# Kernel optimization log

Measured on AMD Instinct MI355X. Metric: run time of the kernel, lower is better.

The kernel has to match this reference:

```python
import jax, jax.numpy as jnp
import numpy as np

B, T, C = 4, 2048, 1024
E, FF, TOPK = 8, 2048, 2


def setup_inputs() -> dict:
    key = jax.random.key(0)
    k1, k2, k3, k4 = jax.random.split(key, 4)
    s_in = 1.0 / np.sqrt(C)
    s_ff = 1.0 / np.sqrt(FF)
    return {
        "x": jax.random.normal(k1, (B, T, C), dtype=jnp.float32),
        "gate_w": jax.random.normal(k2, (E, C), dtype=jnp.float32) * s_in,
        "w1": jax.random.normal(k3, (E, FF, C), dtype=jnp.float32) * s_in,
        "w2": jax.random.normal(k4, (E, C, FF), dtype=jnp.float32) * s_ff,
    }


def reference(x, gate_w, w1, w2):
    Bq, Tq, Cq = x.shape
    x_flat = x.reshape(-1, Cq)                       # [N, C]
    N = x_flat.shape[0]
    scores = x_flat @ gate_w.T                       # [N, E]
    topk_scores, topk_idx = jax.lax.top_k(scores, TOPK)
    topk_probs = jax.nn.softmax(topk_scores, axis=-1)  # [N, K]
    # combine weights per expert: cw[n, e] = sum_k probs[n,k] * (idx[n,k]==e)
    cw = jnp.zeros((N, E), dtype=x_flat.dtype).at[
        jnp.arange(N)[:, None], topk_idx
    ].add(topk_probs)                                # [N, E]
    y = jnp.zeros_like(x_flat)
    for e in range(E):
        h = jax.nn.silu(x_flat @ w1[e].T) @ w2[e].T  # [N, C]
        y = y + cw[:, e:e + 1] * h
    return y.reshape(Bq, Tq, Cq)
```

## Files before the change

kernel.cpp:

```cpp
#include <hip/hip_runtime.h>
#include <hip/hip_bf16.h>
#include <math.h>

#define NTOK 8192
#define CDIM 1024
#define NEXP 8
#define FFD  2048
#define BM   128
#define RMAX (NTOK*2 + NEXP*BM)

typedef __attribute__((ext_vector_type(8))) short short8;
typedef __attribute__((ext_vector_type(4))) float f32x4;

__device__ __forceinline__ unsigned short f2b(float f){
    __hip_bfloat16 b = __float2bfloat16(f);
    return *reinterpret_cast<unsigned short*>(&b);
}
__device__ __forceinline__ float b2f(unsigned short u){
    __hip_bfloat16 b = *reinterpret_cast<__hip_bfloat16*>(&u);
    return __bfloat162float(b);
}

__device__ __forceinline__ void gl_lds16(const void* g, void* l){
    __builtin_amdgcn_global_load_lds(
        (const __attribute__((address_space(1))) unsigned int*)g,
        (__attribute__((address_space(3))) unsigned int*)l, 16, 0, 0);
}

__global__ void k_cvt(const float* __restrict__ src, unsigned short* __restrict__ dst, int n8){
    int i = blockIdx.x*blockDim.x + threadIdx.x;
    if(i >= n8) return;
    const float4* s = reinterpret_cast<const float4*>(src) + (size_t)i*2;
    float4 a = s[0], b = s[1];
    ushort4 o0 = { f2b(a.x), f2b(a.y), f2b(a.z), f2b(a.w) };
    ushort4 o1 = { f2b(b.x), f2b(b.y), f2b(b.z), f2b(b.w) };
    ushort4* d = reinterpret_cast<ushort4*>(dst) + (size_t)i*2;
    d[0] = o0; d[1] = o1;
}

__global__ void k_gate(const float* __restrict__ x, const float* __restrict__ gw,
                       unsigned short* __restrict__ Xb,
                       int* __restrict__ eidx, float* __restrict__ probs){
    int tok  = blockIdx.x*4 + (threadIdx.x>>6);
    int l    = threadIdx.x & 63;
    const float4* xr  = reinterpret_cast<const float4*>(x + (size_t)tok*CDIM);
    ushort4*      xbw = reinterpret_cast<ushort4*>(Xb + (size_t)tok*CDIM);
    float acc[NEXP];
    #pragma unroll
    for(int e=0;e<NEXP;e++) acc[e]=0.f;
    #pragma unroll
    for(int i=0;i<4;i++){
        float4 v = xr[l + 64*i];
        ushort4 o = { f2b(v.x), f2b(v.y), f2b(v.z), f2b(v.w) };
        xbw[l + 64*i] = o;
        #pragma unroll
        for(int e=0;e<NEXP;e++){
            float4 g = reinterpret_cast<const float4*>(gw + e*CDIM)[l + 64*i];
            acc[e] += v.x*g.x + v.y*g.y + v.z*g.z + v.w*g.w;
        }
    }
    #pragma unroll
    for(int e=0;e<NEXP;e++){
        #pragma unroll
        for(int off=32; off; off>>=1) acc[e] += __shfl_xor(acc[e], off);
    }
    if(l==0){
        int e0=0; float s0=acc[0];
        #pragma unroll
        for(int e=1;e<NEXP;e++) if(acc[e]>s0){s0=acc[e]; e0=e;}
        int e1=-1; float s1=-1e30f;
        #pragma unroll
        for(int e=0;e<NEXP;e++) if(e!=e0 && acc[e]>s1){s1=acc[e]; e1=e;}
        float p0 = 1.f/(1.f + expf(s1-s0));
        float p1 = 1.f - p0;
        eidx[2*tok]=e0;  eidx[2*tok+1]=e1;
        probs[2*tok]=p0; probs[2*tok+1]=p1;
    }
}

__global__ void k_rank(const int* __restrict__ eidx, int* __restrict__ slot,
                       int* __restrict__ aoff, int pad){
    __shared__ int run[NEXP];
    __shared__ int wavehist[16][NEXP];
    int tid  = threadIdx.x;
    int lane = tid & 63, w = tid >> 6;
    if(tid < NEXP) run[tid] = 0;
    __syncthreads();
    for(int iter=0; iter<(2*NTOK)/1024; iter++){
        int t = iter*1024 + tid;
        int e = eidx[t];
        unsigned long long mymask = 0;
        #pragma unroll
        for(int ee=0; ee<NEXP; ee++){
            unsigned long long m = __ballot(e==ee);
            if(ee==e) mymask = m;
            if(lane==0) wavehist[w][ee] = __popcll(m);
        }
        int lanerank = __popcll(mymask & ((1ULL<<lane)-1ULL));
        __syncthreads();
        if(tid < NEXP){
            int base = run[tid];
            #pragma unroll
            for(int ww=0; ww<16; ww++){
                int c = wavehist[ww][tid];
                wavehist[ww][tid] = base;
                base += c;
            }
            run[tid] = base;
        }
        __syncthreads();
        slot[t] = wavehist[w][e] + lanerank;
    }
    __syncthreads();
    if(tid==0){
        int off=0;
        for(int e=0;e<NEXP;e++){ aoff[e]=off; off += (run[e]+pad-1)&~(pad-1); }
        aoff[NEXP]=off;
    }
}

__global__ void k_build(const int* __restrict__ eidx, const int* __restrict__ slot,
                        const int* __restrict__ aoff,
                        int* __restrict__ tor, int* __restrict__ row_of){
    int t = blockIdx.x*blockDim.x + threadIdx.x;
    int e = eidx[t];
    int row = aoff[e] + slot[t];
    tor[row] = t>>1;
    row_of[t] = row;
}

template<int KDIM, bool GATHER, bool SILU>
__global__ __launch_bounds__(256, 4)
void k_gemm_fast(const unsigned short* __restrict__ Abase,
                 const int* __restrict__ tor,
                 const unsigned short* __restrict__ zeropg,
                 const unsigned short* __restrict__ Bbase,
                 const int* __restrict__ aoff,
                 unsigned short* __restrict__ Out,
                 int ldo, int bn_rows)
{
    int row0  = blockIdx.x * BM;
    int total = aoff[NEXP];
    if(row0 >= total) return;
    int e = 0;
    while(e < NEXP-1 && row0 >= aoff[e+1]) e++;
    int col0 = blockIdx.y * 128;

    __shared__ unsigned short sA[128*64];
    __shared__ unsigned short sB[128*64];

    int tid = threadIdx.x;
    int l = tid & 63, w = tid >> 6;
    int wr = w >> 1, wc = w & 1;
    int lr = l & 15;

    int sub = l >> 3, c16 = l & 7;
    int csw = (c16 ^ sub) * 16;

    const char* abase[4];
    #pragma unroll
    for(int i=0;i<4;i++){
        int row = w*32 + i*8 + sub;
        if(GATHER){
            int tok = tor[row0 + row];
            abase[i] = (tok>=0) ? (const char*)(Abase + (size_t)tok*KDIM)
                                : (const char*)zeropg;
        } else {
            abase[i] = (const char*)(Abase + (size_t)(row0+row)*KDIM);
        }
        abase[i] += csw;
    }
    const char* Bblk = (const char*)(Bbase + ((size_t)e*bn_rows + col0)*KDIM);
    int boff = (w*32 + sub)*KDIM*2 + csw;

    int kgrp = l >> 4;
    int lsw  = lr & 7;

    f32x4 acc[4][4];
    #pragma unroll
    for(int m=0;m<4;m++)
        #pragma unroll
        for(int n=0;n<4;n++) acc[m][n] = (f32x4){0.f,0.f,0.f,0.f};

    for(int k0=0; k0<KDIM; k0+=64){
        int koff = k0*2;
        #pragma unroll
        for(int i=0;i<4;i++){
            gl_lds16(abase[i]+koff,                      (void*)(sA + (w*4+i)*512));
            gl_lds16(Bblk + boff + i*(8*KDIM*2) + koff,  (void*)(sB + (w*4+i)*512));
        }
        __syncthreads();
        __builtin_amdgcn_s_setprio(1);
        #pragma unroll
        for(int kk=0; kk<2; kk++){
            int swc = ((kk<<2) | kgrp) ^ lsw;
            short8 af[4], bfr[4];
            #pragma unroll
            for(int m=0;m<4;m++)
                af[m] = *reinterpret_cast<const short8*>(sA + (wr*64 + m*16 + lr)*64 + swc*8);
            #pragma unroll
            for(int n=0;n<4;n++)
                bfr[n] = *reinterpret_cast<const short8*>(sB + (wc*64 + n*16 + lr)*64 + swc*8);
            #pragma unroll
            for(int m=0;m<4;m++)
                #pragma unroll
                for(int n=0;n<4;n++)
                    acc[m][n] = __builtin_amdgcn_mfma_f32_16x16x32_bf16(af[m], bfr[n], acc[m][n], 0,0,0);
        }
        __builtin_amdgcn_s_setprio(0);
        __syncthreads();
    }

    int orow_base = row0 + wr*64 + (l>>4)*4;
    int ocol_base = col0 + wc*64 + lr;
    #pragma unroll
    for(int m=0;m<4;m++){
        #pragma unroll
        for(int n=0;n<4;n++){
            f32x4 v = acc[m][n];
            #pragma unroll
            for(int j=0;j<4;j++){
                float val = v[j];
                if(SILU) val = val / (1.f + expf(-val));
                size_t idx = (size_t)(orow_base + m*16 + j)*(size_t)ldo + (size_t)(ocol_base + n*16);
                Out[idx] = f2b(val);
            }
        }
    }
}

__global__ void k_combine(const unsigned short* __restrict__ hout,
                          const int* __restrict__ row_of,
                          const float* __restrict__ probs,
                          float* __restrict__ y){
    int i = blockIdx.x*blockDim.x + threadIdx.x;
    int n  = i >> 7;
    int c8 = (i & 127) * 8;
    int r0 = row_of[2*n], r1 = row_of[2*n+1];
    float p0 = probs[2*n], p1 = probs[2*n+1];
    uint4 h0 = *reinterpret_cast<const uint4*>(hout + (size_t)r0*CDIM + c8);
    uint4 h1 = *reinterpret_cast<const uint4*>(hout + (size_t)r1*CDIM + c8);
    const unsigned short* a = reinterpret_cast<const unsigned short*>(&h0);
    const unsigned short* b = reinterpret_cast<const unsigned short*>(&h1);
    float4 o0, o1;
    o0.x = p0*b2f(a[0]) + p1*b2f(b[0]);
    o0.y = p0*b2f(a[1]) + p1*b2f(b[1]);
    o0.z = p0*b2f(a[2]) + p1*b2f(b[2]);
    o0.w = p0*b2f(a[3]) + p1*b2f(b[3]);
    o1.x = p0*b2f(a[4]) + p1*b2f(b[4]);
    o1.y = p0*b2f(a[5]) + p1*b2f(b[5]);
    o1.z = p0*b2f(a[6]) + p1*b2f(b[6]);
    o1.w = p0*b2f(a[7]) + p1*b2f(b[7]);
    float4* dst = reinterpret_cast<float4*>(y + (size_t)n*CDIM + c8);
    dst[0] = o0; dst[1] = o1;
}

extern "C" void kernel_launch(void* const* d_in, const int* in_sizes, int n_in,
                              void* d_out, int out_size, void* d_ws, size_t ws_size,
                              hipStream_t stream){
    const float* x  = (const float*)d_in[0];
    const float* gw = (const float*)d_in[1];
    const float* w1 = (const float*)d_in[2];
    const float* w2 = (const float*)d_in[3];
    float* y = (float*)d_out;
    char* ws = (char*)d_ws;

    int*   aoff   = (int*)(ws + 64);
    int*   eidx   = (int*)(ws + 256);
    float* probs  = (float*)(ws + 256 + 1*65536);
    int*   slot   = (int*)(ws + 256 + 2*65536);
    int*   row_of = (int*)(ws + 256 + 3*65536);
    int*   tor    = (int*)(ws + 256 + 4*65536);
    unsigned short* zeropg = (unsigned short*)(ws + 512*1024);

    const size_t SZ_XB  = (size_t)NTOK*CDIM*2;
    const size_t SZ_W   = (size_t)NEXP*FFD*CDIM*2;
    const size_t CTRL   = 1<<20;

    unsigned short* Xb   = (unsigned short*)(ws + CTRL);
    unsigned short* W1b  = (unsigned short*)(ws + CTRL + SZ_XB);
    unsigned short* W2b  = (unsigned short*)(ws + CTRL + SZ_XB + SZ_W);
    unsigned short* H    = (unsigned short*)(ws + CTRL + SZ_XB + 2*SZ_W);
    unsigned short* hout = Xb;

    hipMemsetAsync(tor, 0xFF, RMAX*sizeof(int), stream);
    hipMemsetAsync(zeropg, 0, 4096, stream);

    int n8 = NEXP*FFD*CDIM/8;
    k_cvt<<<n8/256, 256, 0, stream>>>(w1, W1b, n8);
    k_cvt<<<n8/256, 256, 0, stream>>>(w2, W2b, n8);
    k_gate<<<NTOK/4, 256, 0, stream>>>(x, gw, Xb, eidx, probs);
    k_rank<<<1, 1024, 0, stream>>>(eidx, slot, aoff, BM);
    k_build<<<NTOK*2/256, 256, 0, stream>>>(eidx, slot, aoff, tor, row_of);

    dim3 g1(RMAX/BM, FFD/128);
    k_gemm_fast<CDIM, true,  true ><<<g1, 256, 0, stream>>>(Xb, tor, zeropg, W1b, aoff, H,    FFD,  FFD);
    dim3 g2(RMAX/BM, CDIM/128);
    k_gemm_fast<FFD,  false, false><<<g2, 256, 0, stream>>>(H,  tor, zeropg, W2b, aoff, hout, CDIM, CDIM);

    k_combine<<<NTOK*CDIM/8/256, 256, 0, stream>>>(hout, row_of, probs, y);
}
```

Measured before the change: 283.6 us.

## Rewrite grouped expert GEMM as 256x256 tiles with double-buffered LDS pipeline

Replaces the 128x128, 256-thread grouped GEMM with a 256x256, 512-thread kernel that double-buffers A and B tiles in 128 KB of LDS. Loads for the next K-steps are issued while MFMAs run on the current stage, controlled by explicit vmcnt waits and barriers. Block indices are remapped so that consecutive workgroups spread across XCDs, and expert padding grows to 256 rows. The aim is better data reuse and hiding of global-load latency. In exchange, larger padding adds wasted rows, and the large LDS footprint limits occupancy.

Result: slower. 312.9 us (+10.3%).

```diff
diff --git a/kernel.cpp b/kernel.cpp
--- a/kernel.cpp
+++ b/kernel.cpp
@@ -6,8 +6,8 @@
 #define CDIM 1024
 #define NEXP 8
 #define FFD  2048
-#define BM   128
-#define RMAX (NTOK*2 + NEXP*BM)
+#define RMAX 18432
+#define NROWT 72
 
 typedef __attribute__((ext_vector_type(8))) short short8;
 typedef __attribute__((ext_vector_type(4))) float f32x4;
@@ -130,99 +130,145 @@
 }
 
 template<int KDIM, bool GATHER, bool SILU>
-__global__ __launch_bounds__(256, 4)
-void k_gemm_fast(const unsigned short* __restrict__ Abase,
-                 const int* __restrict__ tor,
-                 const unsigned short* __restrict__ zeropg,
-                 const unsigned short* __restrict__ Bbase,
-                 const int* __restrict__ aoff,
-                 unsigned short* __restrict__ Out,
-                 int ldo, int bn_rows)
+__global__ __launch_bounds__(512, 2)
+void k_gemm8(const unsigned short* __restrict__ Abase,
+             const int* __restrict__ tor,
+             const unsigned short* __restrict__ zeropg,
+             const unsigned short* __restrict__ Bbase,
+             const int* __restrict__ aoff,
+             unsigned short* __restrict__ Out,
+             int ldo, int bn_rows)
 {
-    int row0  = blockIdx.x * BM;
+    constexpr int NT = KDIM/64;
+    __shared__ unsigned short lds[65536];
+
+    int nblk = gridDim.x, q = nblk >> 3;
+    int wg = (blockIdx.x & 7)*q + (blockIdx.x >> 3);
+    int row_t = wg % NROWT, col_t = wg / NROWT;
+    int row0 = row_t*256, col0 = col_t*256;
     int total = aoff[NEXP];
     if(row0 >= total) return;
     int e = 0;
     while(e < NEXP-1 && row0 >= aoff[e+1]) e++;
-    int col0 = blockIdx.y * 128;
-
-    __shared__ unsigned short sA[128*64];
-    __shared__ unsigned short sB[128*64];
 
     int tid = threadIdx.x;
     int l = tid & 63, w = tid >> 6;
-    int wr = w >> 1, wc = w & 1;
-    int lr = l & 15;
-
+    int wm = w >> 2, wn = w & 3;
+    int lr = l & 15, kgrp = l >> 4, lsw = lr & 7;
     int sub = l >> 3, c16 = l & 7;
     int csw = (c16 ^ sub) * 16;
 
-    const char* abase[4];
-    #pragma unroll
-    for(int i=0;i<4;i++){
-        int row = w*32 + i*8 + sub;
-        if(GATHER){
-            int tok = tor[row0 + row];
-            abase[i] = (tok>=0) ? (const char*)(Abase + (size_t)tok*KDIM)
-                                : (const char*)zeropg;
-        } else {
-            abase[i] = (const char*)(Abase + (size_t)(row0+row)*KDIM);
-        }
-        abase[i] += csw;
+    const char* aptr[4];
+    int bofs[4];
+    #pragma unroll
+    for(int hh=0; hh<2; hh++){
+        #pragma unroll
+        for(int i=0;i<2;i++){
+            int r  = hh*128 + i*64 + w*8 + sub;
+            int id = hh*2+i;
+            if(GATHER){
+                int tok = tor[row0 + r];
+                aptr[id] = (tok>=0) ? (const char*)(Abase + (size_t)tok*KDIM)
+                                    : (const char*)zeropg;
+            } else {
+                aptr[id] = (const char*)(Abase + (size_t)(row0+r)*KDIM);
+            }
+            aptr[id] += csw;
+            bofs[id] = r*KDIM*2 + csw;
+        }
     }
     const char* Bblk = (const char*)(Bbase + ((size_t)e*bn_rows + col0)*KDIM);
-    int boff = (w*32 + sub)*KDIM*2 + csw;
-
-    int kgrp = l >> 4;
-    int lsw  = lr & 7;
-
-    f32x4 acc[4][4];
-    #pragma unroll
-    for(int m=0;m<4;m++)
+
+    auto STAGE = [&](int t, int ht){
+        int base = (t&1)*65536 + ht*16384;
+        #pragma unroll
+        for(int i=0;i<2;i++){
+            char* dst = (char*)lds + base + i*8192 + w*1024;
+            const char* src = (ht>=2) ? (Bblk + bofs[(ht-2)*2+i] + t*128)
+                                      : (aptr[ht*2+i] + t*128);
+            gl_lds16(src, dst);
+        }
+    };
+
+    f32x4 acc[8][4];
+    #pragma unroll
+    for(int m=0;m<8;m++)
         #pragma unroll
         for(int n=0;n<4;n++) acc[m][n] = (f32x4){0.f,0.f,0.f,0.f};
-
-    for(int k0=0; k0<KDIM; k0+=64){
-        int koff = k0*2;
-        #pragma unroll
-        for(int i=0;i<4;i++){
-            gl_lds16(abase[i]+koff,                      (void*)(sA + (w*4+i)*512));
-            gl_lds16(Bblk + boff + i*(8*KDIM*2) + koff,  (void*)(sB + (w*4+i)*512));
-        }
-        __syncthreads();
-        __builtin_amdgcn_s_setprio(1);
-        #pragma unroll
-        for(int kk=0; kk<2; kk++){
-            int swc = ((kk<<2) | kgrp) ^ lsw;
-            short8 af[4], bfr[4];
-            #pragma unroll
-            for(int m=0;m<4;m++)
-                af[m] = *reinterpret_cast<const short8*>(sA + (wr*64 + m*16 + lr)*64 + swc*8);
-            #pragma unroll
-            for(int n=0;n<4;n++)
-                bfr[n] = *reinterpret_cast<const short8*>(sB + (wc*64 + n*16 + lr)*64 + swc*8);
-            #pragma unroll
-            for(int m=0;m<4;m++)
+    short8 bfr[4][2];
+
+    STAGE(0,0); STAGE(0,1); STAGE(0,2); STAGE(0,3);
+    STAGE(1,2); STAGE(1,3);
+    __builtin_amdgcn_sched_barrier(0);
+    asm volatile("s_waitcnt vmcnt(4)");
+    __builtin_amdgcn_sched_barrier(0);
+    __builtin_amdgcn_s_barrier();
+    __builtin_amdgcn_sched_barrier(0);
+
+    for(int t=0; t<NT; ++t){
+        int dbase = (t&1)*65536;
+        #pragma unroll
+        for(int p=0; p<4; ++p){
+            if(p==0){
                 #pragma unroll
                 for(int n=0;n<4;n++)
-                    acc[m][n] = __builtin_amdgcn_mfma_f32_16x16x32_bf16(af[m], bfr[n], acc[m][n], 0,0,0);
-        }
-        __builtin_amdgcn_s_setprio(0);
-        __syncthreads();
-    }
-
-    int orow_base = row0 + wr*64 + (l>>4)*4;
-    int ocol_base = col0 + wc*64 + lr;
-    #pragma unroll
-    for(int m=0;m<4;m++){
+                    #pragma unroll
+                    for(int kk=0;kk<2;kk++){
+                        int rb = wn*64 + n*16 + lr;
+                        int ch = ((kk<<2)|kgrp) ^ lsw;
+                        bfr[n][kk] = *reinterpret_cast<const short8*>(
+                            (const char*)lds + dbase + 32768 + rb*128 + ch*16);
+                    }
+            }
+            short8 af[2][2];
+            #pragma unroll
+            for(int m=0;m<2;m++)
+                #pragma unroll
+                for(int kk=0;kk<2;kk++){
+                    int ra = wm*128 + (p*2+m)*16 + lr;
+                    int ch = ((kk<<2)|kgrp) ^ lsw;
+                    af[m][kk] = *reinterpret_cast<const short8*>(
+                        (const char*)lds + dbase + ra*128 + ch*16);
+                }
+            if(p==0){ if(t+1<NT){ STAGE(t+1,0); STAGE(t+1,1); } }
+            else if(p==1){ if(t+2<NT) STAGE(t+2,2); }
+            else if(p==2){ if(t+2<NT) STAGE(t+2,3); }
+            __builtin_amdgcn_sched_barrier(0);
+            __builtin_amdgcn_s_barrier();
+            __builtin_amdgcn_sched_barrier(0);
+            __builtin_amdgcn_s_setprio(1);
+            #pragma unroll
+            for(int m=0;m<2;m++)
+                #pragma unroll
+                for(int n=0;n<4;n++)
+                    #pragma unroll
+                    for(int kk=0;kk<2;kk++)
+                        acc[p*2+m][n] = __builtin_amdgcn_mfma_f32_16x16x32_bf16(
+                            af[m][kk], bfr[n][kk], acc[p*2+m][n], 0,0,0);
+            __builtin_amdgcn_s_setprio(0);
+            if(p==3){
+                __builtin_amdgcn_sched_barrier(0);
+                if(t < NT-2)       asm volatile("s_waitcnt vmcnt(4)");
+                else if(t == NT-2) asm volatile("s_waitcnt vmcnt(0)");
+            }
+            __builtin_amdgcn_sched_barrier(0);
+            __builtin_amdgcn_s_barrier();
+            __builtin_amdgcn_sched_barrier(0);
+        }
+    }
+
+    int orow = row0 + wm*128 + (l>>4)*4;
+    int ocol = col0 + wn*64 + lr;
+    #pragma unroll
+    for(int mi=0;mi<8;mi++){
         #pragma unroll
         for(int n=0;n<4;n++){
-            f32x4 v = acc[m][n];
+            f32x4 v = acc[mi][n];
             #pragma unroll
             for(int j=0;j<4;j++){
                 float val = v[j];
                 if(SILU) val = val / (1.f + expf(-val));
-                size_t idx = (size_t)(orow_base + m*16 + j)*(size_t)ldo + (size_t)(ocol_base + n*16);
+                size_t idx = (size_t)(orow + mi*16 + j)*(size_t)ldo + (size_t)(ocol + n*16);
                 Out[idx] = f2b(val);
             }
         }
@@ -284,19 +330,17 @@
     unsigned short* hout = Xb;
 
     hipMemsetAsync(tor, 0xFF, RMAX*sizeof(int), stream);
-    hipMemsetAsync(zeropg, 0, 4096, stream);
+    hipMemsetAsync(zeropg, 0, 8192, stream);
 
     int n8 = NEXP*FFD*CDIM/8;
     k_cvt<<<n8/256, 256, 0, stream>>>(w1, W1b, n8);
     k_cvt<<<n8/256, 256, 0, stream>>>(w2, W2b, n8);
     k_gate<<<NTOK/4, 256, 0, stream>>>(x, gw, Xb, eidx, probs);
-    k_rank<<<1, 1024, 0, stream>>>(eidx, slot, aoff, BM);
+    k_rank<<<1, 1024, 0, stream>>>(eidx, slot, aoff, 256);
     k_build<<<NTOK*2/256, 256, 0, stream>>>(eidx, slot, aoff, tor, row_of);
 
-    dim3 g1(RMAX/BM, FFD/128);
-    k_gemm_fast<CDIM, true,  true ><<<g1, 256, 0, stream>>>(Xb, tor, zeropg, W1b, aoff, H,    FFD,  FFD);
-    dim3 g2(RMAX/BM, CDIM/128);
-    k_gemm_fast<FFD,  false, false><<<g2, 256, 0, stream>>>(H,  tor, zeropg, W2b, aoff, hout, CDIM, CDIM);
+    k_gemm8<CDIM, true,  true ><<<NROWT*(FFD/256), 512, 0, stream>>>(Xb, tor, zeropg, W1b, aoff, H,    FFD,  FFD);
+    k_gemm8<FFD,  false, false><<<NROWT*(CDIM/256), 512, 0, stream>>>(H,  tor, zeropg, W2b, aoff, hout, CDIM, CDIM);
 
     k_combine<<<NTOK*CDIM/8/256, 256, 0, stream>>>(hout, row_of, probs, y);
 }
```

## Fuse combine into second GEMM epilogue with atomic adds, merge setup kernels

Applied to the files above, without the earlier changes.

Removes the separate combine kernel. The second expert GEMM now scales each output row by its routing probability and atomically adds it into the fp32 output, which is zeroed with a memset first. The rank and build kernels are merged into one single-block kernel that keeps slots in shared memory and also initializes tor, prow and the zero page, replacing two memsets. The two weight-conversion launches are merged into one. This drops a bf16 intermediate round trip and several launches, at the cost of scattered fp32 atomics, a full-output memset, and a nondeterministic summation order.

After: 315.3 us. +11.2%, slower.

```diff
diff --git a/kernel.cpp b/kernel.cpp
--- a/kernel.cpp
+++ b/kernel.cpp
@@ -16,10 +16,6 @@
     __hip_bfloat16 b = __float2bfloat16(f);
     return *reinterpret_cast<unsigned short*>(&b);
 }
-__device__ __forceinline__ float b2f(unsigned short u){
-    __hip_bfloat16 b = *reinterpret_cast<__hip_bfloat16*>(&u);
-    return __bfloat162float(b);
-}
 
 __device__ __forceinline__ void gl_lds16(const void* g, void* l){
     __builtin_amdgcn_global_load_lds(
@@ -27,14 +23,18 @@
         (__attribute__((address_space(3))) unsigned int*)l, 16, 0, 0);
 }
 
-__global__ void k_cvt(const float* __restrict__ src, unsigned short* __restrict__ dst, int n8){
+__global__ void k_cvt(const float* __restrict__ w1, const float* __restrict__ w2,
+                      unsigned short* __restrict__ W1b, unsigned short* __restrict__ W2b,
+                      int n8){
     int i = blockIdx.x*blockDim.x + threadIdx.x;
-    if(i >= n8) return;
-    const float4* s = reinterpret_cast<const float4*>(src) + (size_t)i*2;
+    const float* src; unsigned short* dst; int j;
+    if(i < n8){ src = w1; dst = W1b; j = i; }
+    else      { src = w2; dst = W2b; j = i - n8; }
+    const float4* s = reinterpret_cast<const float4*>(src) + (size_t)j*2;
     float4 a = s[0], b = s[1];
     ushort4 o0 = { f2b(a.x), f2b(a.y), f2b(a.z), f2b(a.w) };
     ushort4 o1 = { f2b(b.x), f2b(b.y), f2b(b.z), f2b(b.w) };
-    ushort4* d = reinterpret_cast<ushort4*>(dst) + (size_t)i*2;
+    ushort4* d = reinterpret_cast<ushort4*>(dst) + (size_t)j*2;
     d[0] = o0; d[1] = o1;
 }
 
@@ -78,13 +78,18 @@
     }
 }
 
-__global__ void k_rank(const int* __restrict__ eidx, int* __restrict__ slot,
-                       int* __restrict__ aoff, int pad){
+__global__ void k_rankbuild(const int* __restrict__ eidx, const float* __restrict__ probs,
+                            int* __restrict__ aoff,
+                            int* __restrict__ tor, float* __restrict__ prow,
+                            unsigned short* __restrict__ zeropg){
     __shared__ int run[NEXP];
     __shared__ int wavehist[16][NEXP];
+    __shared__ int slot_s[2*NTOK];
     int tid  = threadIdx.x;
     int lane = tid & 63, w = tid >> 6;
     if(tid < NEXP) run[tid] = 0;
+    for(int idx = tid; idx < RMAX; idx += 1024){ tor[idx] = -1; prow[idx] = 0.f; }
+    reinterpret_cast<int*>(zeropg)[tid] = 0;
     __syncthreads();
     for(int iter=0; iter<(2*NTOK)/1024; iter++){
         int t = iter*1024 + tid;
@@ -109,34 +114,34 @@
             run[tid] = base;
         }
         __syncthreads();
-        slot[t] = wavehist[w][e] + lanerank;
+        slot_s[t] = wavehist[w][e] + lanerank;
     }
     __syncthreads();
     if(tid==0){
         int off=0;
-        for(int e=0;e<NEXP;e++){ aoff[e]=off; off += (run[e]+pad-1)&~(pad-1); }
+        for(int e=0;e<NEXP;e++){ aoff[e]=off; off += (run[e]+BM-1)&~(BM-1); }
         aoff[NEXP]=off;
     }
-}
-
-__global__ void k_build(const int* __restrict__ eidx, const int* __restrict__ slot,
-                        const int* __restrict__ aoff,
-                        int* __restrict__ tor, int* __restrict__ row_of){
-    int t = blockIdx.x*blockDim.x + threadIdx.x;
-    int e = eidx[t];
-    int row = aoff[e] + slot[t];
-    tor[row] = t>>1;
-    row_of[t] = row;
-}
-
-template<int KDIM, bool GATHER, bool SILU>
+    __syncthreads();
+    for(int iter=0; iter<(2*NTOK)/1024; iter++){
+        int t = iter*1024 + tid;
+        int e = eidx[t];
+        int row = aoff[e] + slot_s[t];
+        tor[row]  = t>>1;
+        prow[row] = probs[t];
+    }
+}
+
+template<int KDIM, bool GATHER, bool SILU, bool FUSE>
 __global__ __launch_bounds__(256, 4)
 void k_gemm_fast(const unsigned short* __restrict__ Abase,
                  const int* __restrict__ tor,
+                 const float* __restrict__ prow,
                  const unsigned short* __restrict__ zeropg,
                  const unsigned short* __restrict__ Bbase,
                  const int* __restrict__ aoff,
                  unsigned short* __restrict__ Out,
+                 float* __restrict__ yout,
                  int ldo, int bn_rows)
 {
     int row0  = blockIdx.x * BM;
@@ -213,46 +218,38 @@
 
     int orow_base = row0 + wr*64 + (l>>4)*4;
     int ocol_base = col0 + wc*64 + lr;
-    #pragma unroll
-    for(int m=0;m<4;m++){
-        #pragma unroll
-        for(int n=0;n<4;n++){
-            f32x4 v = acc[m][n];
+    if(FUSE){
+        #pragma unroll
+        for(int m=0;m<4;m++){
             #pragma unroll
             for(int j=0;j<4;j++){
-                float val = v[j];
-                if(SILU) val = val / (1.f + expf(-val));
-                size_t idx = (size_t)(orow_base + m*16 + j)*(size_t)ldo + (size_t)(ocol_base + n*16);
-                Out[idx] = f2b(val);
+                int ro = orow_base + m*16 + j;
+                int tkn = tor[ro];
+                float pw = prow[ro];
+                if(tkn >= 0){
+                    float* yrow = yout + (size_t)tkn*CDIM + ocol_base;
+                    #pragma unroll
+                    for(int n=0;n<4;n++)
+                        atomicAdd(yrow + n*16, acc[m][n][j] * pw);
+                }
             }
         }
-    }
-}
-
-__global__ void k_combine(const unsigned short* __restrict__ hout,
-                          const int* __restrict__ row_of,
-                          const float* __restrict__ probs,
-                          float* __restrict__ y){
-    int i = blockIdx.x*blockDim.x + threadIdx.x;
-    int n  = i >> 7;
-    int c8 = (i & 127) * 8;
-    int r0 = row_of[2*n], r1 = row_of[2*n+1];
-    float p0 = probs[2*n], p1 = probs[2*n+1];
-    uint4 h0 = *reinterpret_cast<const uint4*>(hout + (size_t)r0*CDIM + c8);
-    uint4 h1 = *reinterpret_cast<const uint4*>(hout + (size_t)r1*CDIM + c8);
-    const unsigned short* a = reinterpret_cast<const unsigned short*>(&h0);
-    const unsigned short* b = reinterpret_cast<const unsigned short*>(&h1);
-    float4 o0, o1;
-    o0.x = p0*b2f(a[0]) + p1*b2f(b[0]);
-    o0.y = p0*b2f(a[1]) + p1*b2f(b[1]);
-    o0.z = p0*b2f(a[2]) + p1*b2f(b[2]);
-    o0.w = p0*b2f(a[3]) + p1*b2f(b[3]);
-    o1.x = p0*b2f(a[4]) + p1*b2f(b[4]);
-    o1.y = p0*b2f(a[5]) + p1*b2f(b[5]);
-    o1.z = p0*b2f(a[6]) + p1*b2f(b[6]);
-    o1.w = p0*b2f(a[7]) + p1*b2f(b[7]);
-    float4* dst = reinterpret_cast<float4*>(y + (size_t)n*CDIM + c8);
-    dst[0] = o0; dst[1] = o1;
+    } else {
+        #pragma unroll
+        for(int m=0;m<4;m++){
+            #pragma unroll
+            for(int n=0;n<4;n++){
+                f32x4 v = acc[m][n];
+                #pragma unroll
+                for(int j=0;j<4;j++){
+                    float val = v[j];
+                    if(SILU) val = val / (1.f + expf(-val));
+                    size_t idx = (size_t)(orow_base + m*16 + j)*(size_t)ldo + (size_t)(ocol_base + n*16);
+                    Out[idx] = f2b(val);
+                }
+            }
+        }
+    }
 }
 
 extern "C" void kernel_launch(void* const* d_in, const int* in_sizes, int n_in,
@@ -266,12 +263,11 @@
     char* ws = (char*)d_ws;
 
     int*   aoff   = (int*)(ws + 64);
-    int*   eidx   = (int*)(ws + 256);
-    float* probs  = (float*)(ws + 256 + 1*65536);
-    int*   slot   = (int*)(ws + 256 + 2*65536);
-    int*   row_of = (int*)(ws + 256 + 3*65536);
-    int*   tor    = (int*)(ws + 256 + 4*65536);
-    unsigned short* zeropg = (unsigned short*)(ws + 512*1024);
+    int*   eidx   = (int*)(ws + 4096);
+    float* probs  = (float*)(ws + 128*1024);
+    float* prow   = (float*)(ws + 256*1024);
+    int*   tor    = (int*)(ws + 384*1024);
+    unsigned short* zeropg = (unsigned short*)(ws + 768*1024);
 
     const size_t SZ_XB  = (size_t)NTOK*CDIM*2;
     const size_t SZ_W   = (size_t)NEXP*FFD*CDIM*2;
@@ -281,22 +277,18 @@
     unsigned short* W1b  = (unsigned short*)(ws + CTRL + SZ_XB);
     unsigned short* W2b  = (unsigned short*)(ws + CTRL + SZ_XB + SZ_W);
     unsigned short* H    = (unsigned short*)(ws + CTRL + SZ_XB + 2*SZ_W);
-    unsigned short* hout = Xb;
-
-    hipMemsetAsync(tor, 0xFF, RMAX*sizeof(int), stream);
-    hipMemsetAsync(zeropg, 0, 4096, stream);
+
+    hipMemsetAsync(y, 0, (size_t)NTOK*CDIM*sizeof(float), stream);
 
     int n8 = NEXP*FFD*CDIM/8;
-    k_cvt<<<n8/256, 256, 0, stream>>>(w1, W1b, n8);
-    k_cvt<<<n8/256, 256, 0, stream>>>(w2, W2b, n8);
+    k_cvt<<<2*n8/256, 256, 0, stream>>>(w1, w2, W1b, W2b, n8);
     k_gate<<<NTOK/4, 256, 0, stream>>>(x, gw, Xb, eidx, probs);
-    k_rank<<<1, 1024, 0, stream>>>(eidx, slot, aoff, BM);
-    k_build<<<NTOK*2/256, 256, 0, stream>>>(eidx, slot, aoff, tor, row_of);
+    k_rankbuild<<<1, 1024, 0, stream>>>(eidx, probs, aoff, tor, prow, zeropg);
 
     dim3 g1(RMAX/BM, FFD/128);
-    k_gemm_fast<CDIM, true,  true ><<<g1, 256, 0, stream>>>(Xb, tor, zeropg, W1b, aoff, H,    FFD,  FFD);
+    k_gemm_fast<CDIM, true,  true,  false><<<g1, 256, 0, stream>>>(
+        Xb, tor, prow, zeropg, W1b, aoff, H, nullptr, FFD, FFD);
     dim3 g2(RMAX/BM, CDIM/128);
-    k_gemm_fast<FFD,  false, false><<<g2, 256, 0, stream>>>(H,  tor, zeropg, W2b, aoff, hout, CDIM, CDIM);
-
-    k_combine<<<NTOK*CDIM/8/256, 256, 0, stream>>>(hout, row_of, probs, y);
-}
+    k_gemm_fast<FFD,  false, false, true ><<<g2, 256, 0, stream>>>(
+        H,  tor, prow, zeropg, W2b, aoff, nullptr, y, CDIM, CDIM);
+}
```

## Add 256-row GEMM tile with 512 threads for first expert GEMM, merge weight conversions

Applied to the files above, without the earlier changes.

Adds a new grouped GEMM kernel using 256x128 tiles and 8 waves per block, and uses it for the gather+SiLU up-projection. Expert segments are now padded to 256 rows so the larger M-tile can reuse each B tile across more tokens. The two weight fp32->bf16 conversion launches are merged into one. The tradeoff is more padding rows, higher LDS and register use per block, and a loop without double buffering that may lower occupancy.

Measured after the change: 288.5 us. No clear change (+1.7%).

```diff
diff --git a/kernel.cpp b/kernel.cpp
--- a/kernel.cpp
+++ b/kernel.cpp
@@ -6,8 +6,7 @@
 #define CDIM 1024
 #define NEXP 8
 #define FFD  2048
-#define BM   128
-#define RMAX (NTOK*2 + NEXP*BM)
+#define RMAX 18432
 
 typedef __attribute__((ext_vector_type(8))) short short8;
 typedef __attribute__((ext_vector_type(4))) float f32x4;
@@ -27,14 +26,18 @@
         (__attribute__((address_space(3))) unsigned int*)l, 16, 0, 0);
 }
 
-__global__ void k_cvt(const float* __restrict__ src, unsigned short* __restrict__ dst, int n8){
+__global__ void k_cvt(const float* __restrict__ w1, const float* __restrict__ w2,
+                      unsigned short* __restrict__ W1b, unsigned short* __restrict__ W2b,
+                      int n8){
     int i = blockIdx.x*blockDim.x + threadIdx.x;
-    if(i >= n8) return;
-    const float4* s = reinterpret_cast<const float4*>(src) + (size_t)i*2;
+    const float* src; unsigned short* dst; int j;
+    if(i < n8){ src = w1; dst = W1b; j = i; }
+    else      { src = w2; dst = W2b; j = i - n8; }
+    const float4* s = reinterpret_cast<const float4*>(src) + (size_t)j*2;
     float4 a = s[0], b = s[1];
     ushort4 o0 = { f2b(a.x), f2b(a.y), f2b(a.z), f2b(a.w) };
     ushort4 o1 = { f2b(b.x), f2b(b.y), f2b(b.z), f2b(b.w) };
-    ushort4* d = reinterpret_cast<ushort4*>(dst) + (size_t)i*2;
+    ushort4* d = reinterpret_cast<ushort4*>(dst) + (size_t)j*2;
     d[0] = o0; d[1] = o1;
 }
 
@@ -130,6 +133,104 @@
 }
 
 template<int KDIM, bool GATHER, bool SILU>
+__global__ __launch_bounds__(512, 4)
+void k_gemm256(const unsigned short* __restrict__ Abase,
+               const int* __restrict__ tor,
+               const unsigned short* __restrict__ zeropg,
+               const unsigned short* __restrict__ Bbase,
+               const int* __restrict__ aoff,
+               unsigned short* __restrict__ Out,
+               int ldo, int bn_rows)
+{
+    int row0  = blockIdx.x * 256;
+    int total = aoff[NEXP];
+    if(row0 >= total) return;
+    int e = 0;
+    while(e < NEXP-1 && row0 >= aoff[e+1]) e++;
+    int col0 = blockIdx.y * 128;
+
+    __shared__ unsigned short sA[256*64];
+    __shared__ unsigned short sB[128*64];
+
+    int tid = threadIdx.x;
+    int l = tid & 63, w = tid >> 6;
+    int wm = w >> 1, wn = w & 1;
+    int lr = l & 15;
+    int kgrp = l >> 4, lsw = lr & 7;
+    int sub = l >> 3, c16 = l & 7;
+    int csw = (c16 ^ sub) * 16;
+
+    const char* abase[4];
+    #pragma unroll
+    for(int i=0;i<4;i++){
+        int row = (w + 8*i)*8 + sub;
+        if(GATHER){
+            int tok = tor[row0 + row];
+            abase[i] = (tok>=0) ? (const char*)(Abase + (size_t)tok*KDIM)
+                                : (const char*)zeropg;
+        } else {
+            abase[i] = (const char*)(Abase + (size_t)(row0+row)*KDIM);
+        }
+        abase[i] += csw;
+    }
+    const char* Bblk = (const char*)(Bbase + ((size_t)e*bn_rows + col0)*KDIM);
+    int boff = (w*8 + sub)*KDIM*2 + csw;
+
+    f32x4 acc[4][4];
+    #pragma unroll
+    for(int m=0;m<4;m++)
+        #pragma unroll
+        for(int n=0;n<4;n++) acc[m][n] = (f32x4){0.f,0.f,0.f,0.f};
+
+    for(int k0=0; k0<KDIM; k0+=64){
+        int koff = k0*2;
+        #pragma unroll
+        for(int i=0;i<4;i++)
+            gl_lds16(abase[i]+koff, (void*)(sA + (w+8*i)*512));
+        #pragma unroll
+        for(int i=0;i<2;i++)
+            gl_lds16(Bblk + boff + i*(64*KDIM*2) + koff, (void*)(sB + (w+8*i)*512));
+        __syncthreads();
+        __builtin_amdgcn_s_setprio(1);
+        #pragma unroll
+        for(int kk=0; kk<2; kk++){
+            int swc = ((kk<<2) | kgrp) ^ lsw;
+            short8 af[4], bfr[4];
+            #pragma unroll
+            for(int m=0;m<4;m++)
+                af[m] = *reinterpret_cast<const short8*>(sA + (wm*64 + m*16 + lr)*64 + swc*8);
+            #pragma unroll
+            for(int n=0;n<4;n++)
+                bfr[n] = *reinterpret_cast<const short8*>(sB + (wn*64 + n*16 + lr)*64 + swc*8);
+            #pragma unroll
+            for(int m=0;m<4;m++)
+                #pragma unroll
+                for(int n=0;n<4;n++)
+                    acc[m][n] = __builtin_amdgcn_mfma_f32_16x16x32_bf16(af[m], bfr[n], acc[m][n], 0,0,0);
+        }
+        __builtin_amdgcn_s_setprio(0);
+        __syncthreads();
+    }
+
+    int orow_base = row0 + wm*64 + (l>>4)*4;
+    int ocol_base = col0 + wn*64 + lr;
+    #pragma unroll
+    for(int m=0;m<4;m++){
+        #pragma unroll
+        for(int n=0;n<4;n++){
+            f32x4 v = acc[m][n];
+            #pragma unroll
+            for(int j=0;j<4;j++){
+                float val = v[j];
+                if(SILU) val = val / (1.f + expf(-val));
+                size_t idx = (size_t)(orow_base + m*16 + j)*(size_t)ldo + (size_t)(ocol_base + n*16);
+                Out[idx] = f2b(val);
+            }
+        }
+    }
+}
+
+template<int KDIM, bool GATHER, bool SILU>
 __global__ __launch_bounds__(256, 4)
 void k_gemm_fast(const unsigned short* __restrict__ Abase,
                  const int* __restrict__ tor,
@@ -139,7 +240,7 @@
                  unsigned short* __restrict__ Out,
                  int ldo, int bn_rows)
 {
-    int row0  = blockIdx.x * BM;
+    int row0  = blockIdx.x * 128;
     int total = aoff[NEXP];
     if(row0 >= total) return;
     int e = 0;
@@ -153,7 +254,6 @@
     int l = tid & 63, w = tid >> 6;
     int wr = w >> 1, wc = w & 1;
     int lr = l & 15;
-
     int sub = l >> 3, c16 = l & 7;
     int csw = (c16 ^ sub) * 16;
 
@@ -266,12 +366,12 @@
     char* ws = (char*)d_ws;
 
     int*   aoff   = (int*)(ws + 64);
-    int*   eidx   = (int*)(ws + 256);
-    float* probs  = (float*)(ws + 256 + 1*65536);
-    int*   slot   = (int*)(ws + 256 + 2*65536);
-    int*   row_of = (int*)(ws + 256 + 3*65536);
-    int*   tor    = (int*)(ws + 256 + 4*65536);
-    unsigned short* zeropg = (unsigned short*)(ws + 512*1024);
+    int*   eidx   = (int*)(ws + 4096);
+    float* probs  = (float*)(ws + 128*1024);
+    int*   slot   = (int*)(ws + 256*1024);
+    int*   row_of = (int*)(ws + 384*1024);
+    int*   tor    = (int*)(ws + 512*1024);
+    unsigned short* zeropg = (unsigned short*)(ws + 768*1024);
 
     const size_t SZ_XB  = (size_t)NTOK*CDIM*2;
     const size_t SZ_W   = (size_t)NEXP*FFD*CDIM*2;
@@ -287,16 +387,17 @@
     hipMemsetAsync(zeropg, 0, 4096, stream);
 
     int n8 = NEXP*FFD*CDIM/8;
-    k_cvt<<<n8/256, 256, 0, stream>>>(w1, W1b, n8);
-    k_cvt<<<n8/256, 256, 0, stream>>>(w2, W2b, n8);
+    k_cvt<<<2*n8/256, 256, 0, stream>>>(w1, w2, W1b, W2b, n8);
     k_gate<<<NTOK/4, 256, 0, stream>>>(x, gw, Xb, eidx, probs);
-    k_rank<<<1, 1024, 0, stream>>>(eidx, slot, aoff, BM);
+    k_rank<<<1, 1024, 0, stream>>>(eidx, slot, aoff, 256);
     k_build<<<NTOK*2/256, 256, 0, stream>>>(eidx, slot, aoff, tor, row_of);
 
-    dim3 g1(RMAX/BM, FFD/128);
-    k_gemm_fast<CDIM, true,  true ><<<g1, 256, 0, stream>>>(Xb, tor, zeropg, W1b, aoff, H,    FFD,  FFD);
-    dim3 g2(RMAX/BM, CDIM/128);
-    k_gemm_fast<FFD,  false, false><<<g2, 256, 0, stream>>>(H,  tor, zeropg, W2b, aoff, hout, CDIM, CDIM);
+    dim3 g1(RMAX/256, FFD/128);
+    k_gemm256<CDIM, true, true><<<g1, 512, 0, stream>>>(
+        Xb, tor, zeropg, W1b, aoff, H, FFD, FFD);
+    dim3 g2(RMAX/128, CDIM/128);
+    k_gemm_fast<FFD, false, false><<<g2, 256, 0, stream>>>(
+        H, tor, zeropg, W2b, aoff, hout, CDIM, CDIM);
 
     k_combine<<<NTOK*CDIM/8/256, 256, 0, stream>>>(hout, row_of, probs, y);
 }
```
